# Kernel tuning notes

Hardware: AMD Instinct MI355X
Metric: run time of the kernel (lower is better)

## Reference

```python
import jax, jax.numpy as jnp
import numpy as np

N = 1024
DH = 64   # XH feature dim (<= DOUT)
DP = 32   # XP feature dim
DIN = 64  # input_dim (== output_dim, required by f_psi applied to vij)
DOUT = 64 # output_dim
BN_EPS = 1e-5
SIGMA = 0.1


def setup_inputs() -> dict:
    key = jax.random.key(0)
    ks = jax.random.split(key, 8)
    return {
        "XH": jax.random.normal(ks[0], (N, DH), dtype=jnp.float32),
        "XP": jax.random.normal(ks[1], (N, DP), dtype=jnp.float32),
        "XX": jax.random.normal(ks[2], (N, DIN), dtype=jnp.float32),
        "K": 16,
        # nn.Parameter weight/bias: normal(0, 0.01)
        "weight": 0.01 * jax.random.normal(ks[3], (DIN, DOUT), dtype=jnp.float32),
        "bias": 0.01 * jax.random.normal(ks[4], (DOUT,), dtype=jnp.float32),
        # f_psi Linear params (torch kaiming-uniform ~ small uniform)
        "psi_w": jax.random.uniform(ks[5], (DOUT, DIN), dtype=jnp.float32, minval=-1.0, maxval=1.0) / np.sqrt(DIN),
        "psi_b": jax.random.uniform(ks[6], (DOUT,), dtype=jnp.float32, minval=-1.0, maxval=1.0) / np.sqrt(DIN),
        # BatchNorm1d affine params
        "gamma": jnp.ones((DOUT,), dtype=jnp.float32),
        "beta": jnp.zeros((DOUT,), dtype=jnp.float32),
    }


def _pairwise_norm(X):
    # [N, N] matrix of L2 norms of row differences (as in torch.norm(X[:,None]-X, dim=2))
    return jnp.linalg.norm(X[:, None, :] - X[None, :, :], axis=2)


def _adjacency(XH, XP, K, sigma=SIGMA):
    eps = float(np.finfo(np.float64).eps)
    XHs = XH / (sigma + eps)
    WHo = _pairwise_norm(XHs)
    WH = jnp.exp(-((WHo - WHo.min()) / (WHo.max() - WHo.min())) / 2)
    Wlo = _pairwise_norm(XP)
    Wl = jnp.exp(-((Wlo - Wlo.min()) / (Wlo.max() - Wlo.min())))
    WW = WH + 0.2 * Wl
    _, idx = jax.lax.top_k(WW, K)                       # per-row top-K neighbors
    n = WW.shape[0]
    mask = jnp.zeros_like(WW).at[jnp.arange(n)[:, None], idx].set(1.0)
    mask = mask + mask.T                                # symmetrize
    # Original sets Adj=WW/WW=1 where mask!=0 and Adj=WW-WW=0 elsewhere -> binary adjacency
    return (mask > 0).astype(WW.dtype)


def reference(XH, XP, XX, K, weight, bias, psi_w, psi_b, gamma, beta):
    Adj = _adjacency(XH, XP, K)                         # [N, N], {0,1}
    x = XX @ weight                                     # [N, D]
    vi = x[None, :, :] * Adj[:, :, None]                # [N, N, D]: vi[i,j] = x[j]*Adj[i,j]
    vij = x[None, :, :] + vi                            # [N, N, D]
    # f_psi: Linear -> BatchNorm1d (training-mode batch stats) -> Sigmoid, over N*N rows
    h = jnp.einsum('ijd,ed->ije', vij, psi_w) + psi_b   # [N, N, D]
    mu = h.mean(axis=(0, 1))                            # [D]
    var = h.var(axis=(0, 1))                            # biased var, as torch BN
    att = jax.nn.sigmoid((h - mu) * jax.lax.rsqrt(var + BN_EPS) * gamma + beta)
    # self-loop attention forced to 1 on the diagonal
    eye = jnp.eye(x.shape[0], dtype=bool)[:, :, None]
    att = jnp.where(eye, jnp.float32(1.0), att)
    out = (att * vi).sum(axis=0) + bias                 # [N, D]
    return (out[:, :XH.shape[1]], XP, out)
```

## Files before the change

### kernel.cpp

```cpp
#include <hip/hip_runtime.h>
#include <cfloat>

#define NN 1024


__global__ __launch_bounds__(256) void gcn_transpose(const float* __restrict__ XH,
                                                     const float* __restrict__ XP,
                                                     float* __restrict__ XHT,
                                                     float* __restrict__ XPT,
                                                     unsigned* __restrict__ maxbits,
                                                     double* __restrict__ Sbins) {
    const int b = blockIdx.x;
    const int j0 = b * 64;
    const int tid = threadIdx.x;
    Sbins[b * 256 + tid] = 0.0;
    if (b == 0 && tid < 64) maxbits[tid] = 0u;
    __shared__ float th[64][65];
    __shared__ float tp[32][65];
#pragma unroll
    for (int it = 0; it < 16; ++it) {
        int idx = it * 256 + tid;
        int jl = idx >> 6, d = idx & 63;
        th[d][jl] = XH[(j0 + jl) * 64 + d];
    }
#pragma unroll
    for (int it = 0; it < 8; ++it) {
        int idx = it * 256 + tid;
        int jl = idx >> 5, d = idx & 31;
        tp[d][jl] = XP[(j0 + jl) * 32 + d];
    }
    __syncthreads();
#pragma unroll
    for (int it = 0; it < 16; ++it) {
        int idx = it * 256 + tid;
        int d = idx >> 6, jl = idx & 63;
        XHT[d * NN + j0 + jl] = th[d][jl];
    }
#pragma unroll
    for (int it = 0; it < 8; ++it) {
        int idx = it * 256 + tid;
        int d = idx >> 6, jl = idx & 63;
        XPT[d * NN + j0 + jl] = tp[d][jl];
    }
}

__global__ __launch_bounds__(256) void gcn_dist(const float* __restrict__ XH,
                                                const float* __restrict__ XP,
                                                const float* __restrict__ XHT,
                                                const float* __restrict__ XPT,
                                                float* __restrict__ dhp,
                                                float* __restrict__ dpp,
                                                unsigned* __restrict__ maxbits,
                                                const int* __restrict__ kptr,
                                                int* __restrict__ cdeg) {
    const int b = blockIdx.x;
    const int i0 = (b >> 2) * 4;
    const int j = (b & 3) * 256 + threadIdx.x;
    const int tid = threadIdx.x;
    if (b < 4) cdeg[j] = *kptr;
    __shared__ float shi[4][64];
    __shared__ float spi[4][32];
    shi[tid >> 6][tid & 63] = XH[(i0 + (tid >> 6)) * 64 + (tid & 63)];
    if (tid < 128) spi[tid >> 5][tid & 31] = XP[(i0 + (tid >> 5)) * 32 + (tid & 31)];
    __syncthreads();
    float dh[4] = {0.f, 0.f, 0.f, 0.f}, dp[4] = {0.f, 0.f, 0.f, 0.f};
#pragma unroll 16
    for (int d = 0; d < 64; ++d) {
        float v = XHT[d * NN + j];
#pragma unroll
        for (int r = 0; r < 4; ++r) { float t = v - shi[r][d]; dh[r] += t * t; }
    }
#pragma unroll 16
    for (int d = 0; d < 32; ++d) {
        float v = XPT[d * NN + j];
#pragma unroll
        for (int r = 0; r < 4; ++r) { float t = v - spi[r][d]; dp[r] += t * t; }
    }
#pragma unroll
    for (int r = 0; r < 4; ++r) {
        dhp[(size_t)(i0 + r) * NN + j] = sqrtf(dh[r]);
        dpp[(size_t)(i0 + r) * NN + j] = sqrtf(dp[r]);
    }
    float mh = fmaxf(fmaxf(dh[0], dh[1]), fmaxf(dh[2], dh[3]));
    float mp = fmaxf(fmaxf(dp[0], dp[1]), fmaxf(dp[2], dp[3]));
#pragma unroll
    for (int m = 1; m < 64; m <<= 1) {
        mh = fmaxf(mh, __shfl_xor(mh, m));
        mp = fmaxf(mp, __shfl_xor(mp, m));
    }
    __shared__ float wmx[4][2];
    if ((tid & 63) == 0) { wmx[tid >> 6][0] = mh; wmx[tid >> 6][1] = mp; }
    __syncthreads();
    if (tid == 0) {
        float a = fmaxf(fmaxf(wmx[0][0], wmx[1][0]), fmaxf(wmx[2][0], wmx[3][0]));
        float b2 = fmaxf(fmaxf(wmx[0][1], wmx[1][1]), fmaxf(wmx[2][1], wmx[3][1]));
        atomicMax(&maxbits[0], __float_as_uint(a));
        atomicMax(&maxbits[32], __float_as_uint(b2));
    }
}

__global__ __launch_bounds__(256) void gcn_topk(const float* __restrict__ dhp,
                                                const float* __restrict__ dpp,
                                                const unsigned* __restrict__ maxbits,
                                                const int* __restrict__ kptr,
                                                int* __restrict__ eidx,
                                                int* __restrict__ cdeg) {
    const int tid = threadIdx.x;
    const int w = tid >> 6, lane = tid & 63;
    const int i = blockIdx.x * 4 + w;
    const float cH = -0.5f / sqrtf(__uint_as_float(maxbits[0]));
    const float cP = -1.0f / sqrtf(__uint_as_float(maxbits[32]));
    const float4* dh4 = (const float4*)(dhp + (size_t)i * NN);
    const float4* dp4 = (const float4*)(dpp + (size_t)i * NN);
    unsigned long long kk[16];
#pragma unroll
    for (int s = 0; s < 4; ++s) {
        float4 a = dh4[s * 64 + lane];
        float4 b = dp4[s * 64 + lane];
        float w0 = __expf(a.x * cH) + 0.2f * __expf(b.x * cP);
        float w1 = __expf(a.y * cH) + 0.2f * __expf(b.y * cP);
        float w2 = __expf(a.z * cH) + 0.2f * __expf(b.z * cP);
        float w3 = __expf(a.w * cH) + 0.2f * __expf(b.w * cP);
        int jb = s * 256 + lane * 4;
        kk[s * 4 + 0] = ((unsigned long long)__float_as_uint(w0) << 32) | (unsigned)(1023 - (jb + 0));
        kk[s * 4 + 1] = ((unsigned long long)__float_as_uint(w1) << 32) | (unsigned)(1023 - (jb + 1));
        kk[s * 4 + 2] = ((unsigned long long)__float_as_uint(w2) << 32) | (unsigned)(1023 - (jb + 2));
        kk[s * 4 + 3] = ((unsigned long long)__float_as_uint(w3) << 32) | (unsigned)(1023 - (jb + 3));
    }
    const int K = *kptr;
    int jsave = 0;
    for (int t = 0; t < K; ++t) {
        unsigned long long bk = 0ull;
#pragma unroll
        for (int v = 0; v < 16; ++v) bk = kk[v] > bk ? kk[v] : bk;
#pragma unroll
        for (int m = 1; m < 64; m <<= 1) {
            unsigned long long o = __shfl_xor(bk, m);
            bk = o > bk ? o : bk;
        }
        int j = 1023 - (int)(bk & 0x3FFull);
        if (lane == t) jsave = j;
        if (((j >> 2) & 63) == lane) {
            int slot = ((j >> 8) << 2) | (j & 3);
#pragma unroll
            for (int v = 0; v < 16; ++v)
                if (v == slot) kk[v] = 0ull;
        }
    }
    if (lane < K) {
        eidx[i * 16 + lane] = jsave;
        atomicAdd(&cdeg[jsave], 1);
    }
}

__global__ __launch_bounds__(256) void gcn_overlap(const int* __restrict__ eidx,
                                                   int* __restrict__ cdeg) {
    const int gid = blockIdx.x * 256 + threadIdx.x;
    const int i = gid >> 4;
    const int j = eidx[gid];
    if (j < 0) return;
    const int4* ej = (const int4*)(eidx + j * 16);
    bool rec = false;
#pragma unroll
    for (int q = 0; q < 4; ++q) {
        int4 e = ej[q];
        rec |= (e.x == i) | (e.y == i) | (e.z == i) | (e.w == i);
    }
    if (rec) atomicSub(&cdeg[j], 1);
}

__global__ __launch_bounds__(64) void gcn_xy(const float* __restrict__ XX,
                                             const float* __restrict__ W,
                                             const float* __restrict__ psi_w,
                                             const int* __restrict__ cdeg,
                                             float* __restrict__ x,
                                             float* __restrict__ y,
                                             double* __restrict__ S1,
                                             double* __restrict__ S2) {
    const int i = blockIdx.x;
    const int e = threadIdx.x;
    __shared__ float xin[64], xs[64];
    xin[e] = XX[i * 64 + e];
    __syncthreads();
    float acc = 0.f;
#pragma unroll
    for (int d = 0; d < 64; ++d) acc += xin[d] * W[d * 64 + e];
    xs[e] = acc;
    x[i * 64 + e] = acc;
    __syncthreads();
    float acc2 = 0.f;
    const float* pw = psi_w + e * 64;
#pragma unroll
    for (int d = 0; d < 64; ++d) acc2 += xs[d] * pw[d];
    y[i * 64 + e] = acc2;
    const int c = cdeg[i];
    const int bin = (i & 31) * 64 + e;
    double yd = (double)acc2;
    atomicAdd(&S1[bin], (double)(NN + c) * yd);
    atomicAdd(&S2[bin], (double)(NN + 3 * c) * yd * yd);
}

__global__ __launch_bounds__(64) void gcn_statsfin(const double* __restrict__ S1,
                                                   const double* __restrict__ S2,
                                                   const float* __restrict__ gamma,
                                                   float* __restrict__ m0,
                                                   float* __restrict__ scale) {
    const int e = threadIdx.x;
    double s1 = 0.0, s2 = 0.0;
#pragma unroll
    for (int b = 0; b < 32; ++b) { s1 += S1[b * 64 + e]; s2 += S2[b * 64 + e]; }
    double m = s1 / 1048576.0;
    double var = s2 / 1048576.0 - m * m;
    m0[e] = (float)m;
    scale[e] = (float)(1.0 / sqrt(var + 1e-5)) * gamma[e];
}

__global__ __launch_bounds__(64) void gcn_out(const float* __restrict__ x,
                                              const float* __restrict__ y,
                                              const int* __restrict__ cdeg,
                                              const float* __restrict__ beta,
                                              const float* __restrict__ m0,
                                              const float* __restrict__ scale,
                                              const float* __restrict__ bias,
                                              const float* __restrict__ XP,
                                              float* __restrict__ out) {
    const int j = blockIdx.x;
    const int e = threadIdx.x;
    float t = y[j * 64 + e];
    float z = (2.f * t - m0[e]) * scale[e] + beta[e];
    float s = 1.f / (1.f + expf(-z));
    float val = x[j * 64 + e] * ((float)(cdeg[j] - 1) * s + 1.f) + bias[e];
    out[j * 64 + e] = val;
    out[98304 + j * 64 + e] = val;
    if (e < 32) out[65536 + j * 32 + e] = XP[j * 32 + e];
}

extern "C" void kernel_launch(void* const* d_in, const int* in_sizes, int n_in,
                              void* d_out, int out_size, void* d_ws, size_t ws_size,
                              hipStream_t stream) {
    const float* XH    = (const float*)d_in[0];
    const float* XP    = (const float*)d_in[1];
    const float* XX    = (const float*)d_in[2];
    const int*   Kp    = (const int*)d_in[3];
    const float* W     = (const float*)d_in[4];
    const float* bias  = (const float*)d_in[5];
    const float* psi_w = (const float*)d_in[6];
    const float* psi_b = (const float*)d_in[7];
    const float* gamma = (const float*)d_in[8];
    const float* beta  = (const float*)d_in[9];
    (void)psi_b;
    float* out = (float*)d_out;
    char* ws = (char*)d_ws;

    float* dhp        = (float*)ws;
    float* dpp        = (float*)(ws + 0x400000);
    float* XHT        = (float*)(ws + 0x800000);
    float* XPT        = (float*)(ws + 0x840000);
    int* eidx         = (int*)(ws + 0x860000);
    unsigned* maxbits = (unsigned*)(ws + 0x870000);
    int* cdeg         = (int*)(ws + 0x871000);
    double* S1        = (double*)(ws + 0x872000);
    double* S2        = (double*)(ws + 0x876000);
    float* m0         = (float*)(ws + 0x87A000);
    float* scale      = (float*)(ws + 0x87A200);
    float* x          = (float*)(ws + 0x880000);
    float* y          = (float*)(ws + 0x8C0000);

    gcn_transpose<<<dim3(16), dim3(256), 0, stream>>>(XH, XP, XHT, XPT, maxbits, S1);
    gcn_dist<<<dim3(1024), dim3(256), 0, stream>>>(XH, XP, XHT, XPT, dhp, dpp, maxbits, Kp, cdeg);
    gcn_topk<<<dim3(256), dim3(256), 0, stream>>>(dhp, dpp, maxbits, Kp, eidx, cdeg);
    gcn_overlap<<<dim3(64), dim3(256), 0, stream>>>(eidx, cdeg);
    gcn_xy<<<dim3(1024), dim3(64), 0, stream>>>(XX, W, psi_w, cdeg, x, y, S1, S2);
    gcn_statsfin<<<dim3(1), dim3(64), 0, stream>>>(S1, S2, gamma, m0, scale);
    gcn_out<<<dim3(1024), dim3(64), 0, stream>>>(x, y, cdeg, beta, m0, scale, bias, XP, out);
}
```

Baseline: 144.3 us.

## Fuse prep kernels, replace atomic max with per-block maxima, merge stats finalize

Combines the transpose, x/y projection, and workspace initialization into one multi-role prep kernel. The global atomicMax is replaced by per-block max writes that topk reduces itself. BN stats finalization is folded into the output kernel, and launches are widened to 256 threads. The aims are fewer launches, less serialization on launch overhead and atomic contention, and the x/y work overlapping with the transpose. In exchange, every output block redundantly recomputes the stats reduction and every topk block re-reduces 1024 maxima.

```diff
diff --git a/kernel.cpp b/kernel.cpp
--- a/kernel.cpp
+++ b/kernel.cpp
@@ -4,43 +4,76 @@
 #define NN 1024
 
 
-__global__ __launch_bounds__(256) void gcn_transpose(const float* __restrict__ XH,
-                                                     const float* __restrict__ XP,
-                                                     float* __restrict__ XHT,
-                                                     float* __restrict__ XPT,
-                                                     unsigned* __restrict__ maxbits,
-                                                     double* __restrict__ Sbins) {
+__global__ __launch_bounds__(256) void gcn_prep(const float* __restrict__ XH,
+                                                const float* __restrict__ XP,
+                                                const float* __restrict__ XX,
+                                                const float* __restrict__ W,
+                                                const float* __restrict__ psi_w,
+                                                const int* __restrict__ kptr,
+                                                float* __restrict__ XHT,
+                                                float* __restrict__ XPT,
+                                                float* __restrict__ x,
+                                                float* __restrict__ y,
+                                                double* __restrict__ Sbins,
+                                                int* __restrict__ cdeg) {
     const int b = blockIdx.x;
-    const int j0 = b * 64;
     const int tid = threadIdx.x;
-    Sbins[b * 256 + tid] = 0.0;
-    if (b == 0 && tid < 64) maxbits[tid] = 0u;
     __shared__ float th[64][65];
     __shared__ float tp[32][65];
-#pragma unroll
-    for (int it = 0; it < 16; ++it) {
-        int idx = it * 256 + tid;
-        int jl = idx >> 6, d = idx & 63;
-        th[d][jl] = XH[(j0 + jl) * 64 + d];
-    }
-#pragma unroll
-    for (int it = 0; it < 8; ++it) {
-        int idx = it * 256 + tid;
-        int jl = idx >> 5, d = idx & 31;
-        tp[d][jl] = XP[(j0 + jl) * 32 + d];
-    }
-    __syncthreads();
-#pragma unroll
-    for (int it = 0; it < 16; ++it) {
-        int idx = it * 256 + tid;
-        int d = idx >> 6, jl = idx & 63;
-        XHT[d * NN + j0 + jl] = th[d][jl];
-    }
-#pragma unroll
-    for (int it = 0; it < 8; ++it) {
-        int idx = it * 256 + tid;
-        int d = idx >> 6, jl = idx & 63;
-        XPT[d * NN + j0 + jl] = tp[d][jl];
+    __shared__ float xybuf[4][2][64];
+    if (b < 16) {
+        const int j0 = b * 64;
+#pragma unroll
+        for (int it = 0; it < 16; ++it) {
+            int idx = it * 256 + tid;
+            int jl = idx >> 6, d = idx & 63;
+            th[d][jl] = XH[(j0 + jl) * 64 + d];
+        }
+#pragma unroll
+        for (int it = 0; it < 8; ++it) {
+            int idx = it * 256 + tid;
+            int jl = idx >> 5, d = idx & 31;
+            tp[d][jl] = XP[(j0 + jl) * 32 + d];
+        }
+        __syncthreads();
+#pragma unroll
+        for (int it = 0; it < 16; ++it) {
+            int idx = it * 256 + tid;
+            int d = idx >> 6, jl = idx & 63;
+            XHT[d * NN + j0 + jl] = th[d][jl];
+        }
+#pragma unroll
+        for (int it = 0; it < 8; ++it) {
+            int idx = it * 256 + tid;
+            int d = idx >> 6, jl = idx & 63;
+            XPT[d * NN + j0 + jl] = tp[d][jl];
+        }
+    } else if (b < 80) {
+        const int w = tid >> 6, e = tid & 63;
+        const int ibase = (b - 16) * 16 + w * 4;
+#pragma unroll
+        for (int r = 0; r < 4; ++r) {
+            const int i = ibase + r;
+            xybuf[w][0][e] = XX[i * 64 + e];
+            __syncthreads();
+            float acc = 0.f;
+#pragma unroll
+            for (int d = 0; d < 64; ++d) acc += xybuf[w][0][d] * W[d * 64 + e];
+            x[i * 64 + e] = acc;
+            xybuf[w][1][e] = acc;
+            __syncthreads();
+            float acc2 = 0.f;
+            const float* pw = psi_w + e * 64;
+#pragma unroll
+            for (int d = 0; d < 64; ++d) acc2 += xybuf[w][1][d] * pw[d];
+            y[i * 64 + e] = acc2;
+        }
+    } else {
+        const int K = *kptr;
+#pragma unroll
+        for (int k = 0; k < 16; ++k) Sbins[tid * 16 + k] = 0.0;
+#pragma unroll
+        for (int q = 0; q < 4; ++q) cdeg[q * 256 + tid] = K;
     }
 }
 
@@ -50,14 +83,11 @@
                                                 const float* __restrict__ XPT,
                                                 float* __restrict__ dhp,
                                                 float* __restrict__ dpp,
-                                                unsigned* __restrict__ maxbits,
-                                                const int* __restrict__ kptr,
-                                                int* __restrict__ cdeg) {
+                                                float2* __restrict__ bmax) {
     const int b = blockIdx.x;
     const int i0 = (b >> 2) * 4;
     const int j = (b & 3) * 256 + threadIdx.x;
     const int tid = threadIdx.x;
-    if (b < 4) cdeg[j] = *kptr;
     __shared__ float shi[4][64];
     __shared__ float spi[4][32];
     shi[tid >> 6][tid & 63] = XH[(i0 + (tid >> 6)) * 64 + (tid & 63)];
@@ -94,22 +124,37 @@
     if (tid == 0) {
         float a = fmaxf(fmaxf(wmx[0][0], wmx[1][0]), fmaxf(wmx[2][0], wmx[3][0]));
         float b2 = fmaxf(fmaxf(wmx[0][1], wmx[1][1]), fmaxf(wmx[2][1], wmx[3][1]));
-        atomicMax(&maxbits[0], __float_as_uint(a));
-        atomicMax(&maxbits[32], __float_as_uint(b2));
+        bmax[b] = make_float2(a, b2);
     }
 }
 
 __global__ __launch_bounds__(256) void gcn_topk(const float* __restrict__ dhp,
                                                 const float* __restrict__ dpp,
-                                                const unsigned* __restrict__ maxbits,
+                                                const float2* __restrict__ bmax,
                                                 const int* __restrict__ kptr,
                                                 int* __restrict__ eidx,
                                                 int* __restrict__ cdeg) {
     const int tid = threadIdx.x;
     const int w = tid >> 6, lane = tid & 63;
     const int i = blockIdx.x * 4 + w;
-    const float cH = -0.5f / sqrtf(__uint_as_float(maxbits[0]));
-    const float cP = -1.0f / sqrtf(__uint_as_float(maxbits[32]));
+    float mh = 0.f, mp = 0.f;
+#pragma unroll
+    for (int q = 0; q < 4; ++q) {
+        float2 v = bmax[q * 256 + tid];
+        mh = fmaxf(mh, v.x); mp = fmaxf(mp, v.y);
+    }
+#pragma unroll
+    for (int m = 1; m < 64; m <<= 1) {
+        mh = fmaxf(mh, __shfl_xor(mh, m));
+        mp = fmaxf(mp, __shfl_xor(mp, m));
+    }
+    __shared__ float warr[4][2];
+    if (lane == 0) { warr[w][0] = mh; warr[w][1] = mp; }
+    __syncthreads();
+    mh = fmaxf(fmaxf(warr[0][0], warr[1][0]), fmaxf(warr[2][0], warr[3][0]));
+    mp = fmaxf(fmaxf(warr[0][1], warr[1][1]), fmaxf(warr[2][1], warr[3][1]));
+    const float cH = -0.5f / sqrtf(mh);
+    const float cP = -1.0f / sqrtf(mp);
     const float4* dh4 = (const float4*)(dhp + (size_t)i * NN);
     const float4* dp4 = (const float4*)(dpp + (size_t)i * NN);
     unsigned long long kk[16];
@@ -169,65 +214,40 @@
     if (rec) atomicSub(&cdeg[j], 1);
 }
 
-__global__ __launch_bounds__(64) void gcn_xy(const float* __restrict__ XX,
-                                             const float* __restrict__ W,
-                                             const float* __restrict__ psi_w,
-                                             const int* __restrict__ cdeg,
-                                             float* __restrict__ x,
-                                             float* __restrict__ y,
-                                             double* __restrict__ S1,
-                                             double* __restrict__ S2) {
-    const int i = blockIdx.x;
-    const int e = threadIdx.x;
-    __shared__ float xin[64], xs[64];
-    xin[e] = XX[i * 64 + e];
-    __syncthreads();
-    float acc = 0.f;
-#pragma unroll
-    for (int d = 0; d < 64; ++d) acc += xin[d] * W[d * 64 + e];
-    xs[e] = acc;
-    x[i * 64 + e] = acc;
-    __syncthreads();
-    float acc2 = 0.f;
-    const float* pw = psi_w + e * 64;
-#pragma unroll
-    for (int d = 0; d < 64; ++d) acc2 += xs[d] * pw[d];
-    y[i * 64 + e] = acc2;
-    const int c = cdeg[i];
-    const int bin = (i & 31) * 64 + e;
-    double yd = (double)acc2;
+__global__ __launch_bounds__(256) void gcn_stats(const float* __restrict__ y,
+                                                 const int* __restrict__ cdeg,
+                                                 double* __restrict__ S1,
+                                                 double* __restrict__ S2) {
+    const int w = threadIdx.x >> 6, e = threadIdx.x & 63;
+    const int j = blockIdx.x * 4 + w;
+    const int c = cdeg[j];
+    const double yd = (double)y[j * 64 + e];
+    const int bin = (j & 31) * 64 + e;
     atomicAdd(&S1[bin], (double)(NN + c) * yd);
     atomicAdd(&S2[bin], (double)(NN + 3 * c) * yd * yd);
 }
 
-__global__ __launch_bounds__(64) void gcn_statsfin(const double* __restrict__ S1,
-                                                   const double* __restrict__ S2,
-                                                   const float* __restrict__ gamma,
-                                                   float* __restrict__ m0,
-                                                   float* __restrict__ scale) {
-    const int e = threadIdx.x;
+__global__ __launch_bounds__(256) void gcn_out(const float* __restrict__ x,
+                                               const float* __restrict__ y,
+                                               const int* __restrict__ cdeg,
+                                               const float* __restrict__ gamma,
+                                               const float* __restrict__ beta,
+                                               const double* __restrict__ S1,
+                                               const double* __restrict__ S2,
+                                               const float* __restrict__ bias,
+                                               const float* __restrict__ XP,
+                                               float* __restrict__ out) {
+    const int w = threadIdx.x >> 6, e = threadIdx.x & 63;
+    const int j = blockIdx.x * 4 + w;
     double s1 = 0.0, s2 = 0.0;
 #pragma unroll
     for (int b = 0; b < 32; ++b) { s1 += S1[b * 64 + e]; s2 += S2[b * 64 + e]; }
-    double m = s1 / 1048576.0;
-    double var = s2 / 1048576.0 - m * m;
-    m0[e] = (float)m;
-    scale[e] = (float)(1.0 / sqrt(var + 1e-5)) * gamma[e];
-}
-
-__global__ __launch_bounds__(64) void gcn_out(const float* __restrict__ x,
-                                              const float* __restrict__ y,
-                                              const int* __restrict__ cdeg,
-                                              const float* __restrict__ beta,
-                                              const float* __restrict__ m0,
-                                              const float* __restrict__ scale,
-                                              const float* __restrict__ bias,
-                                              const float* __restrict__ XP,
-                                              float* __restrict__ out) {
-    const int j = blockIdx.x;
-    const int e = threadIdx.x;
+    const double m = s1 / 1048576.0;
+    const double var = s2 / 1048576.0 - m * m;
+    const float m0e = (float)m;
+    const float scalee = (float)(1.0 / sqrt(var + 1e-5)) * gamma[e];
     float t = y[j * 64 + e];
-    float z = (2.f * t - m0[e]) * scale[e] + beta[e];
+    float z = (2.f * t - m0e) * scalee + beta[e];
     float s = 1.f / (1.f + expf(-z));
     float val = x[j * 64 + e] * ((float)(cdeg[j] - 1) * s + 1.f) + bias[e];
     out[j * 64 + e] = val;
@@ -252,25 +272,22 @@
     float* out = (float*)d_out;
     char* ws = (char*)d_ws;
 
-    float* dhp        = (float*)ws;
-    float* dpp        = (float*)(ws + 0x400000);
-    float* XHT        = (float*)(ws + 0x800000);
-    float* XPT        = (float*)(ws + 0x840000);
-    int* eidx         = (int*)(ws + 0x860000);
-    unsigned* maxbits = (unsigned*)(ws + 0x870000);
-    int* cdeg         = (int*)(ws + 0x871000);
-    double* S1        = (double*)(ws + 0x872000);
-    double* S2        = (double*)(ws + 0x876000);
-    float* m0         = (float*)(ws + 0x87A000);
-    float* scale      = (float*)(ws + 0x87A200);
-    float* x          = (float*)(ws + 0x880000);
-    float* y          = (float*)(ws + 0x8C0000);
-
-    gcn_transpose<<<dim3(16), dim3(256), 0, stream>>>(XH, XP, XHT, XPT, maxbits, S1);
-    gcn_dist<<<dim3(1024), dim3(256), 0, stream>>>(XH, XP, XHT, XPT, dhp, dpp, maxbits, Kp, cdeg);
-    gcn_topk<<<dim3(256), dim3(256), 0, stream>>>(dhp, dpp, maxbits, Kp, eidx, cdeg);
+    float* dhp   = (float*)ws;
+    float* dpp   = (float*)(ws + 0x400000);
+    float* XHT   = (float*)(ws + 0x800000);
+    float* XPT   = (float*)(ws + 0x840000);
+    int* eidx    = (int*)(ws + 0x860000);
+    float2* bmax = (float2*)(ws + 0x870000);
+    int* cdeg    = (int*)(ws + 0x872000);
+    double* S1   = (double*)(ws + 0x874000);
+    double* S2   = (double*)(ws + 0x878000);
+    float* x     = (float*)(ws + 0x880000);
+    float* y     = (float*)(ws + 0x8C0000);
+
+    gcn_prep<<<dim3(81), dim3(256), 0, stream>>>(XH, XP, XX, W, psi_w, Kp, XHT, XPT, x, y, S1, cdeg);
+    gcn_dist<<<dim3(1024), dim3(256), 0, stream>>>(XH, XP, XHT, XPT, dhp, dpp, bmax);
+    gcn_topk<<<dim3(256), dim3(256), 0, stream>>>(dhp, dpp, bmax, Kp, eidx, cdeg);
     gcn_overlap<<<dim3(64), dim3(256), 0, stream>>>(eidx, cdeg);
-    gcn_xy<<<dim3(1024), dim3(64), 0, stream>>>(XX, W, psi_w, cdeg, x, y, S1, S2);
-    gcn_statsfin<<<dim3(1), dim3(64), 0, stream>>>(S1, S2, gamma, m0, scale);
-    gcn_out<<<dim3(1024), dim3(64), 0, stream>>>(x, y, cdeg, beta, m0, scale, bias, XP, out);
-}
+    gcn_stats<<<dim3(256), dim3(256), 0, stream>>>(y, cdeg, S1, S2);
+    gcn_out<<<dim3(256), dim3(256), 0, stream>>>(x, y, cdeg, gamma, beta, S1, S2, bias, XP, out);
+}
```

Measured after the change: 147.1 us. No clear change (+2.0%).
